# Performance work log

Hardware: AMD Instinct MI355X
Metric: run time of the kernel (lower is better)

Reference implementation:

```python
import jax, jax.numpy as jnp
import numpy as np

H = 128          # rnn_hid_size
SEQ_LEN = 2048
B = 4096
IN = 2           # SELECT_SIZE * 2


def _uniform(key, shape, stdv):
    return jax.random.uniform(key, shape, jnp.float32, -stdv, stdv)


def setup_inputs() -> dict:
    key = jax.random.key(0)
    ks = jax.random.split(key, 20)
    values = jax.random.normal(ks[0], (B, SEQ_LEN, 3), jnp.float32)
    masks = (jax.random.uniform(ks[1], (B, SEQ_LEN)) > 0.5).astype(jnp.float32)
    deltas = jax.random.uniform(ks[2], (B, SEQ_LEN, 3), jnp.float32)
    eval_masks = (jax.random.uniform(ks[3], (B, SEQ_LEN)) > 0.5).astype(jnp.float32)
    s = 1.0 / np.sqrt(H)
    params = {
        'Wih0': _uniform(ks[4], (4 * H, IN), s), 'Whh0': _uniform(ks[5], (4 * H, H), s),
        'bih0': _uniform(ks[6], (4 * H,), s), 'bhh0': _uniform(ks[7], (4 * H,), s),
        'Wih1': _uniform(ks[8], (4 * H, IN), s), 'Whh1': _uniform(ks[9], (4 * H, H), s),
        'bih1': _uniform(ks[10], (4 * H,), s), 'bhh1': _uniform(ks[11], (4 * H,), s),
        'td_W': _uniform(ks[12], (H, 1), s), 'td_b': _uniform(ks[13], (H,), s),
        'hr_W': _uniform(ks[14], (1, H), 1.0 / np.sqrt(H)), 'hr_b': _uniform(ks[15], (1,), 1.0 / np.sqrt(H)),
    }
    return dict(values=values, masks=masks, deltas=deltas, eval_masks=eval_masks, **params)


def _lstm_cell(x, h, c, Wih, Whh, bih, bhh):
    g = x @ Wih.T + bih + h @ Whh.T + bhh            # [B, 4H]
    i, f, gg, o = jnp.split(g, 4, axis=1)
    c2 = jax.nn.sigmoid(f) * c + jax.nn.sigmoid(i) * jnp.tanh(gg)
    h2 = jax.nn.sigmoid(o) * jnp.tanh(c2)
    return h2, c2


def reference(values, masks, deltas, eval_masks,
              Wih0, Whh0, bih0, bhh0, Wih1, Whh1, bih1, bhh1,
              td_W, td_b, hr_W, hr_b):
    bsize = values.shape[0]
    # time-major sequences for scan
    x_seq = jnp.transpose(values[:, :, 2:3], (1, 0, 2))      # [T, B, 1]
    m_seq = jnp.transpose(masks[:, :, None], (1, 0, 2))      # [T, B, 1]
    d_seq = jnp.transpose(deltas[:, :, 2:3], (1, 0, 2))      # [T, B, 1]
    in1_seq = jnp.transpose(values[:, :, 0:2], (1, 0, 2))    # [T, B, 2]

    h0 = jnp.zeros((bsize, H), jnp.float32)
    h1 = jnp.zeros((bsize, H), jnp.float32)
    c1 = jnp.zeros((bsize, H), jnp.float32)
    loss0 = jnp.zeros((), jnp.float32)

    def step(carry, inp):
        h0, h1, c1, loss = carry
        x_y, m_y, d_y, in1 = inp
        gamma_h = jnp.exp(-jax.nn.relu(d_y @ td_W.T + td_b))  # [B, H]
        x_h = h0 @ hr_W.T + hr_b                              # [B, 1]
        x_c = m_y * x_y + (1.0 - m_y) * x_h
        loss = loss + jnp.sum(jnp.square(x_y - x_h) * m_y) / (jnp.sum(m_y) + 1e-05)
        h1n, c1n = _lstm_cell(in1, h1, c1, Wih1, Whh1, bih1, bhh1)
        h1n = h1n * gamma_h
        inputs = jnp.concatenate([x_c, m_y], axis=1)          # [B, 2]
        h0n, _ = _lstm_cell(inputs, h1n, c1n, Wih0, Whh0, bih0, bhh0)
        return (h0n, h1n, c1n, loss), x_c

    (_, _, _, loss), imp = jax.lax.scan(step, (h0, h1, c1, loss0),
                                        (x_seq, m_seq, d_seq, in1_seq))
    imputations = jnp.transpose(imp, (1, 0, 2))               # [B, T, 1]
    evals = values[:, :, 2:3]
    return (loss, imputations, eval_masks[:, :, None], evals, masks[:, :, None])
```

## Files before the change

### kernel.cpp

```cpp
#include <hip/hip_runtime.h>

typedef __attribute__((ext_vector_type(8))) short bf16x8;
typedef __attribute__((ext_vector_type(4))) float f32x4;

#define L2E 1.4426950408889634f

__device__ __forceinline__ short f2bf(float x){
  unsigned u = __builtin_bit_cast(unsigned, x);
  u += 0x7fffu + ((u >> 16) & 1u);
  return (short)(u >> 16);
}
__device__ __forceinline__ float sigm(float x){
  float e = __builtin_amdgcn_exp2f(-x * L2E);
  return __builtin_amdgcn_rcpf(1.0f + e);
}
__device__ __forceinline__ float tanh_(float x){
  float e = __builtin_amdgcn_exp2f(x * (2.0f * L2E));
  return 1.0f - 2.0f * __builtin_amdgcn_rcpf(1.0f + e);
}

__device__ __forceinline__ void wg_barrier(){
  asm volatile("s_waitcnt lgkmcnt(0)" ::: "memory");
  __builtin_amdgcn_s_barrier();
  asm volatile("" ::: "memory");
}

__global__ __launch_bounds__(512, 2)
void rios_main(const float* __restrict__ values, const float* __restrict__ masks,
               const float* __restrict__ deltas,
               const float* __restrict__ Wih0, const float* __restrict__ Whh0,
               const float* __restrict__ bih0, const float* __restrict__ bhh0,
               const float* __restrict__ Wih1, const float* __restrict__ Whh1,
               const float* __restrict__ bih1, const float* __restrict__ bhh1,
               const float* __restrict__ td_W, const float* __restrict__ td_b,
               const float* __restrict__ hr_W, const float* __restrict__ hr_b,
               float* __restrict__ out, float* __restrict__ lossws)
{
  __shared__ short hb[2][16][136];
  __shared__ float xh_part[2][8][16];
  __shared__ float sA[2][5][16][16];
  __shared__ float xh_hist[16][16];

  const int tid = threadIdx.x;
  const int w  = tid >> 6;
  const int l  = tid & 63;
  const int q  = l >> 4;
  const int c  = l & 15;
  const int q4 = q << 2;
  const int u  = (w << 4) + c;
  const long long bb = (long long)blockIdx.x * 16;

  bf16x8 wf[2][4][4];
  {
    const float* WhhA[2] = { Whh1, Whh0 };
    #pragma unroll
    for (int cell = 0; cell < 2; ++cell)
      #pragma unroll
      for (int gi = 0; gi < 4; ++gi)
        #pragma unroll
        for (int kt = 0; kt < 4; ++kt){
          const float* rp = WhhA[cell] + (((gi << 7) + u) << 7) + (kt << 5) + (q << 3);
          bf16x8 f;
          #pragma unroll
          for (int j = 0; j < 8; ++j) f[j] = f2bf(rp[j]);
          wf[cell][gi][kt] = f;
        }
  }
  float wi[2][4][2], bs[2][4];
  {
    const float* WihA[2] = { Wih1, Wih0 };
    const float* bihA[2] = { bih1, bih0 };
    const float* bhhA[2] = { bhh1, bhh0 };
    #pragma unroll
    for (int cell = 0; cell < 2; ++cell)
      #pragma unroll
      for (int gi = 0; gi < 4; ++gi){
        int rg = (gi << 7) + u;
        wi[cell][gi][0] = WihA[cell][rg * 2];
        wi[cell][gi][1] = WihA[cell][rg * 2 + 1];
        bs[cell][gi]    = bihA[cell][rg] + bhhA[cell][rg];
      }
  }
  const float tdw = td_W[u], tdbv = td_b[u], hrw = hr_W[u], hrb = hr_b[0];

  {
    short* hz = &hb[0][0][0];
    for (int i = tid; i < 16 * 136; i += 512) hz[i] = 0;
    if (tid < 256) ((float*)xh_part)[tid] = 0.f;
  }

  const int isV = (tid < 192);
  const int isD = (tid >= 192 && tid < 384);
  const int isM = (tid >= 384 && tid < 448);
  int lb = 0, lp = 0;
  if (isV){ lb = tid / 12;        lp = tid % 12; }
  else if (isD){ lb = (tid-192)/12; lp = (tid-192)%12; }
  else if (isM){ lb = (tid-384)/4;  lp = (tid-384)%4; }
  const float* ldbase = nullptr;
  if (isV)      ldbase = values + ((bb + lb) * 2048LL) * 3 + lp * 4;
  else if (isD) ldbase = deltas + ((bb + lb) * 2048LL) * 3 + lp * 4;
  else if (isM) ldbase = masks  +  (bb + lb) * 2048LL      + lp * 4;

  auto write_stage = [&](int buf, f32x4 r){
    if (isV){
      #pragma unroll
      for (int j = 0; j < 4; ++j){ int idx = lp * 4 + j; sA[buf][idx % 3][idx / 3][lb] = r[j]; }
    } else if (isD){
      #pragma unroll
      for (int j = 0; j < 4; ++j){ int idx = lp * 4 + j; if (idx % 3 == 2) sA[buf][4][idx / 3][lb] = r[j]; }
    } else if (isM){
      #pragma unroll
      for (int j = 0; j < 4; ++j){ sA[buf][3][lp * 4 + j][lb] = r[j]; }
    }
  };

  if (tid < 448){
    f32x4 st = *(const f32x4*)(ldbase);
    write_stage(0, st);
  }
  __syncthreads();

  f32x4 c1 = {0.f, 0.f, 0.f, 0.f};

  for (int cc = 0; cc < 128; ++cc){
    const int cb = cc & 1;
    f32x4 nst;
    #pragma unroll 1
    for (int tt = 0; tt < 16; ++tt){
      const int s = (cc << 4) + tt;
      const int p = tt & 1;
      const int ob  = (tt == 0) ? (cb ^ 1) : cb;
      const int ott = (tt == 0) ? 15 : (tt - 1);

      if (w == 0 && tt == 1 && cc > 0){
        const int obase = (cc - 1) << 4;
        const int pb = cb ^ 1;
        const int m = l >> 2, j = l & 3;
        f32x4 st, wse, sm;
        #pragma unroll
        for (int k = 0; k < 4; ++k){
          const int t2 = (j << 2) + k;
          float xy2 = sA[pb][2][t2][m];
          float mm2 = sA[pb][3][t2][m];
          float xh2 = xh_hist[t2][m];
          st[k]  = mm2 * xy2 + (1.f - mm2) * xh2;
          float d2 = xy2 - xh2;
          wse[k] = d2 * d2 * mm2;
          sm[k]  = mm2;
        }
        *((f32x4*)&out[1 + (bb + m) * 2048LL + obase + (j << 2)]) = st;
        #pragma unroll
        for (int mk = 4; mk <= 32; mk <<= 1){
          #pragma unroll
          for (int k = 0; k < 4; ++k){ wse[k] += __shfl_xor(wse[k], mk); sm[k] += __shfl_xor(sm[k], mk); }
        }
        if (l < 4){
          #pragma unroll
          for (int k = 0; k < 4; ++k){
            atomicAdd(&lossws[((obase + (j << 2) + k) << 1)    ], wse[k]);
            atomicAdd(&lossws[((obase + (j << 2) + k) << 1) + 1], sm[k]);
          }
        }
      }

      f32x4 v0v = *(const f32x4*)&sA[cb][0][tt][q4];
      f32x4 v1v = *(const f32x4*)&sA[cb][1][tt][q4];
      f32x4 dv  = *(const f32x4*)&sA[cb][4][tt][q4];
      f32x4 acc[4];
      #pragma unroll
      for (int gi = 0; gi < 4; ++gi){
        #pragma unroll
        for (int r = 0; r < 4; ++r)
          acc[gi][r] = fmaf(v0v[r], wi[0][gi][0], fmaf(v1v[r], wi[0][gi][1], bs[0][gi]));
      }
      #pragma unroll
      for (int kt = 0; kt < 4; ++kt){
        bf16x8 af = *(const bf16x8*)&hb[p][c][(kt << 5) + (q << 3)];
        #pragma unroll
        for (int gi = 0; gi < 4; ++gi)
          acc[gi] = __builtin_amdgcn_mfma_f32_16x16x32_bf16(af, wf[0][gi][kt], acc[gi], 0, 0, 0);
      }

      f32x4 xh = { hrb, hrb, hrb, hrb };
      #pragma unroll
      for (int w2 = 0; w2 < 8; ++w2)
        xh += *(const f32x4*)&xh_part[p][w2][q4];
      f32x4 xy = *(const f32x4*)&sA[ob][2][ott][q4];
      f32x4 mm = *(const f32x4*)&sA[ob][3][ott][q4];
      f32x4 xcv = mm * xy + (1.f - mm) * xh;
      if (w == 0 && c == 0 && s > 0) *((f32x4*)&xh_hist[ott][q4]) = xh;

      f32x4 c_old = c1;
      #pragma unroll
      for (int r = 0; r < 4; ++r){
        float si = sigm(acc[0][r]);
        float sf = sigm(acc[1][r]);
        float tg = tanh_(acc[2][r]);
        float so = sigm(acc[3][r]);
        float c2 = sf * c1[r] + si * tg;
        float a1 = fmaxf(fmaf(dv[r], tdw, tdbv), 0.f);
        float gam = __builtin_amdgcn_exp2f(-a1 * L2E);
        c1[r] = c2;
        hb[p ^ 1][q4 + r][u] = f2bf(so * tanh_(c2) * gam);
      }

      #pragma unroll
      for (int gi = 0; gi < 4; ++gi){
        #pragma unroll
        for (int r = 0; r < 4; ++r)
          acc[gi][r] = fmaf(xcv[r], wi[1][gi][0], fmaf(mm[r], wi[1][gi][1], bs[1][gi]));
      }
      #pragma unroll
      for (int kt = 0; kt < 4; ++kt){
        bf16x8 af = *(const bf16x8*)&hb[p][c][(kt << 5) + (q << 3)];
        #pragma unroll
        for (int gi = 0; gi < 4; ++gi)
          acc[gi] = __builtin_amdgcn_mfma_f32_16x16x32_bf16(af, wf[1][gi][kt], acc[gi], 0, 0, 0);
      }
      f32x4 pv;
      #pragma unroll
      for (int r = 0; r < 4; ++r){
        float si = sigm(acc[0][r]);
        float sf = sigm(acc[1][r]);
        float tg = tanh_(acc[2][r]);
        float so = sigm(acc[3][r]);
        float c0n = sf * c_old[r] + si * tg;
        pv[r] = so * tanh_(c0n) * hrw;
      }
      #pragma unroll
      for (int mk = 1; mk < 16; mk <<= 1){
        #pragma unroll
        for (int r = 0; r < 4; ++r) pv[r] += __shfl_xor(pv[r], mk);
      }
      if (c == 0 && s > 0) *((f32x4*)&xh_part[p ^ 1][w][q4]) = pv;

      if (tt == 12 && cc + 1 < 128 && tid < 448){
        long long t0 = (long long)(cc + 1) * 16;
        nst = *(const f32x4*)(ldbase + (isM ? t0 : t0 * 3));
      }
      if (tt == 15 && cc + 1 < 128 && tid < 448) write_stage(cb ^ 1, nst);

      wg_barrier();
    }
  }

  if (w == 0){
    f32x4 xh = { hrb, hrb, hrb, hrb };
    #pragma unroll
    for (int w2 = 0; w2 < 8; ++w2)
      xh += *(const f32x4*)&xh_part[0][w2][q4];
    if (c == 0) *((f32x4*)&xh_hist[15][q4]) = xh;
    asm volatile("s_waitcnt lgkmcnt(0)" ::: "memory");
    const int obase = 2032;
    const int m = l >> 2, j = l & 3;
    f32x4 st, wse, sm;
    #pragma unroll
    for (int k = 0; k < 4; ++k){
      const int t2 = (j << 2) + k;
      float xy2 = sA[1][2][t2][m];
      float mm2 = sA[1][3][t2][m];
      float xh2 = xh_hist[t2][m];
      st[k]  = mm2 * xy2 + (1.f - mm2) * xh2;
      float d2 = xy2 - xh2;
      wse[k] = d2 * d2 * mm2;
      sm[k]  = mm2;
    }
    *((f32x4*)&out[1 + (bb + m) * 2048LL + obase + (j << 2)]) = st;
    #pragma unroll
    for (int mk = 4; mk <= 32; mk <<= 1){
      #pragma unroll
      for (int k = 0; k < 4; ++k){ wse[k] += __shfl_xor(wse[k], mk); sm[k] += __shfl_xor(sm[k], mk); }
    }
    if (l < 4){
      #pragma unroll
      for (int k = 0; k < 4; ++k){
        atomicAdd(&lossws[((obase + (j << 2) + k) << 1)    ], wse[k]);
        atomicAdd(&lossws[((obase + (j << 2) + k) << 1) + 1], sm[k]);
      }
    }
  }
}

__global__ void loss_reduce(const float* __restrict__ lossws, float* __restrict__ out){
  __shared__ float red[1024];
  int t = threadIdx.x;
  float v = lossws[2 * t] / (lossws[2 * t + 1] + 1e-5f)
          + lossws[2 * (t + 1024)] / (lossws[2 * (t + 1024) + 1] + 1e-5f);
  red[t] = v;
  __syncthreads();
  for (int s = 512; s > 0; s >>= 1){
    if (t < s) red[t] += red[t + s];
    __syncthreads();
  }
  if (t == 0) out[0] = red[0];
}

__global__ void copy_outs(const float* __restrict__ values, const float* __restrict__ masks,
                          const float* __restrict__ evalm, float* __restrict__ out){
  const long long M = 8388608LL;
  long long i = (long long)blockIdx.x * 256 + threadIdx.x;
  if (i < M){
    out[1 + M     + i] = evalm[i];
    out[1 + 2 * M + i] = values[3 * i + 2];
    out[1 + 3 * M + i] = masks[i];
  }
}

extern "C" void kernel_launch(void* const* d_in, const int* in_sizes, int n_in,
                              void* d_out, int out_size, void* d_ws, size_t ws_size,
                              hipStream_t stream){
  const float* values = (const float*)d_in[0];
  const float* masks  = (const float*)d_in[1];
  const float* deltas = (const float*)d_in[2];
  const float* evalm  = (const float*)d_in[3];
  const float* Wih0   = (const float*)d_in[4];
  const float* Whh0   = (const float*)d_in[5];
  const float* bih0   = (const float*)d_in[6];
  const float* bhh0   = (const float*)d_in[7];
  const float* Wih1   = (const float*)d_in[8];
  const float* Whh1   = (const float*)d_in[9];
  const float* bih1   = (const float*)d_in[10];
  const float* bhh1   = (const float*)d_in[11];
  const float* td_W   = (const float*)d_in[12];
  const float* td_b   = (const float*)d_in[13];
  const float* hr_W   = (const float*)d_in[14];
  const float* hr_b   = (const float*)d_in[15];
  float* out    = (float*)d_out;
  float* lossws = (float*)d_ws;

  hipMemsetAsync(lossws, 0, 2048 * 2 * sizeof(float), stream);
  hipLaunchKernelGGL(copy_outs, dim3(32768), dim3(256), 0, stream, values, masks, evalm, out);
  hipLaunchKernelGGL(rios_main, dim3(256), dim3(512), 0, stream,
                     values, masks, deltas, Wih0, Whh0, bih0, bhh0,
                     Wih1, Whh1, bih1, bhh1, td_W, td_b, hr_W, hr_b, out, lossws);
  hipLaunchKernelGGL(loss_reduce, dim3(1), dim3(1024), 0, stream, lossws, out);
}
```

Baseline: 10.13 ms.

## Split the two LSTM cells across separate wave groups running concurrently

The block grows to 1024 threads. Waves 0-7 now compute the time-decayed layer-1 cell and waves 8-15 compute the skewed layer-0 cell, instead of every wave doing both cells one after the other. The layer-1 cell state is passed through a new double-buffered LDS array so the other group can read it a step later. Each wave now holds only one cell's weight fragments, which lowers register pressure and halves the serial MFMA and transcendental chain per step. In exchange, twice as many waves join each per-step barrier, and the block's LDS footprint grows.

New measurement: 12.05 ms. +19.0%, slower.

```diff
diff --git a/kernel.cpp b/kernel.cpp
--- a/kernel.cpp
+++ b/kernel.cpp
@@ -25,7 +25,7 @@
   asm volatile("" ::: "memory");
 }
 
-__global__ __launch_bounds__(512, 2)
+__global__ __launch_bounds__(1024, 4)
 void rios_main(const float* __restrict__ values, const float* __restrict__ masks,
                const float* __restrict__ deltas,
                const float* __restrict__ Wih0, const float* __restrict__ Whh0,
@@ -37,55 +37,56 @@
                float* __restrict__ out, float* __restrict__ lossws)
 {
   __shared__ short hb[2][16][136];
+  __shared__ float cst[2][16][132];
   __shared__ float xh_part[2][8][16];
   __shared__ float sA[2][5][16][16];
   __shared__ float xh_hist[16][16];
 
   const int tid = threadIdx.x;
-  const int w  = tid >> 6;
-  const int l  = tid & 63;
-  const int q  = l >> 4;
-  const int c  = l & 15;
-  const int q4 = q << 2;
-  const int u  = (w << 4) + c;
+  const int w   = tid >> 6;
+  const int grp = w >> 3;
+  const int wg  = w & 7;
+  const int l   = tid & 63;
+  const int q   = l >> 4;
+  const int c   = l & 15;
+  const int q4  = q << 2;
+  const int u   = (wg << 4) + c;
   const long long bb = (long long)blockIdx.x * 16;
 
-  bf16x8 wf[2][4][4];
-  {
-    const float* WhhA[2] = { Whh1, Whh0 };
+  const float* Whh = grp == 0 ? Whh1 : Whh0;
+  const float* Wih = grp == 0 ? Wih1 : Wih0;
+  const float* bih = grp == 0 ? bih1 : bih0;
+  const float* bhh = grp == 0 ? bhh1 : bhh0;
+
+  bf16x8 wf[4][4];
+  #pragma unroll
+  for (int gi = 0; gi < 4; ++gi)
     #pragma unroll
-    for (int cell = 0; cell < 2; ++cell)
-      #pragma unroll
-      for (int gi = 0; gi < 4; ++gi)
-        #pragma unroll
-        for (int kt = 0; kt < 4; ++kt){
-          const float* rp = WhhA[cell] + (((gi << 7) + u) << 7) + (kt << 5) + (q << 3);
-          bf16x8 f;
-          #pragma unroll
-          for (int j = 0; j < 8; ++j) f[j] = f2bf(rp[j]);
-          wf[cell][gi][kt] = f;
-        }
-  }
-  float wi[2][4][2], bs[2][4];
-  {
-    const float* WihA[2] = { Wih1, Wih0 };
-    const float* bihA[2] = { bih1, bih0 };
-    const float* bhhA[2] = { bhh1, bhh0 };
-    #pragma unroll
-    for (int cell = 0; cell < 2; ++cell)
-      #pragma unroll
-      for (int gi = 0; gi < 4; ++gi){
-        int rg = (gi << 7) + u;
-        wi[cell][gi][0] = WihA[cell][rg * 2];
-        wi[cell][gi][1] = WihA[cell][rg * 2 + 1];
-        bs[cell][gi]    = bihA[cell][rg] + bhhA[cell][rg];
-      }
-  }
-  const float tdw = td_W[u], tdbv = td_b[u], hrw = hr_W[u], hrb = hr_b[0];
+    for (int kt = 0; kt < 4; ++kt){
+      const float* rp = Whh + (((gi << 7) + u) << 7) + (kt << 5) + (q << 3);
+      bf16x8 f;
+      #pragma unroll
+      for (int j = 0; j < 8; ++j) f[j] = f2bf(rp[j]);
+      wf[gi][kt] = f;
+    }
+  float wi[4][2], bs[4];
+  #pragma unroll
+  for (int gi = 0; gi < 4; ++gi){
+    int rg = (gi << 7) + u;
+    wi[gi][0] = Wih[rg * 2];
+    wi[gi][1] = Wih[rg * 2 + 1];
+    bs[gi]    = bih[rg] + bhh[rg];
+  }
+  float tdw = 0.f, tdbv = 0.f, hrw = 0.f;
+  if (grp == 0){ tdw = td_W[u]; tdbv = td_b[u]; }
+  else         { hrw = hr_W[u]; }
+  const float hrb = hr_b[0];
 
   {
     short* hz = &hb[0][0][0];
-    for (int i = tid; i < 16 * 136; i += 512) hz[i] = 0;
+    for (int i = tid; i < 16 * 136; i += 1024) hz[i] = 0;
+    float* cz = &cst[0][0][0];
+    for (int i = tid; i < 16 * 132; i += 1024) cz[i] = 0.f;
     if (tid < 256) ((float*)xh_part)[tid] = 0.f;
   }
 
@@ -132,107 +133,109 @@
       const int ob  = (tt == 0) ? (cb ^ 1) : cb;
       const int ott = (tt == 0) ? 15 : (tt - 1);
 
-      if (w == 0 && tt == 1 && cc > 0){
-        const int obase = (cc - 1) << 4;
-        const int pb = cb ^ 1;
-        const int m = l >> 2, j = l & 3;
-        f32x4 st, wse, sm;
-        #pragma unroll
-        for (int k = 0; k < 4; ++k){
-          const int t2 = (j << 2) + k;
-          float xy2 = sA[pb][2][t2][m];
-          float mm2 = sA[pb][3][t2][m];
-          float xh2 = xh_hist[t2][m];
-          st[k]  = mm2 * xy2 + (1.f - mm2) * xh2;
-          float d2 = xy2 - xh2;
-          wse[k] = d2 * d2 * mm2;
-          sm[k]  = mm2;
-        }
-        *((f32x4*)&out[1 + (bb + m) * 2048LL + obase + (j << 2)]) = st;
-        #pragma unroll
-        for (int mk = 4; mk <= 32; mk <<= 1){
-          #pragma unroll
-          for (int k = 0; k < 4; ++k){ wse[k] += __shfl_xor(wse[k], mk); sm[k] += __shfl_xor(sm[k], mk); }
-        }
-        if (l < 4){
+      if (grp == 0){
+        f32x4 v0v = *(const f32x4*)&sA[cb][0][tt][q4];
+        f32x4 v1v = *(const f32x4*)&sA[cb][1][tt][q4];
+        f32x4 dv  = *(const f32x4*)&sA[cb][4][tt][q4];
+        f32x4 acc[4];
+        #pragma unroll
+        for (int gi = 0; gi < 4; ++gi){
+          #pragma unroll
+          for (int r = 0; r < 4; ++r)
+            acc[gi][r] = fmaf(v0v[r], wi[gi][0], fmaf(v1v[r], wi[gi][1], bs[gi]));
+        }
+        #pragma unroll
+        for (int kt = 0; kt < 4; ++kt){
+          bf16x8 af = *(const bf16x8*)&hb[p][c][(kt << 5) + (q << 3)];
+          #pragma unroll
+          for (int gi = 0; gi < 4; ++gi)
+            acc[gi] = __builtin_amdgcn_mfma_f32_16x16x32_bf16(af, wf[gi][kt], acc[gi], 0, 0, 0);
+        }
+        #pragma unroll
+        for (int r = 0; r < 4; ++r){
+          float si = sigm(acc[0][r]);
+          float sf = sigm(acc[1][r]);
+          float tg = tanh_(acc[2][r]);
+          float so = sigm(acc[3][r]);
+          float c2 = sf * c1[r] + si * tg;
+          float a1 = fmaxf(fmaf(dv[r], tdw, tdbv), 0.f);
+          float gam = __builtin_amdgcn_exp2f(-a1 * L2E);
+          c1[r] = c2;
+          hb [p ^ 1][q4 + r][u] = f2bf(so * tanh_(c2) * gam);
+          cst[p ^ 1][q4 + r][u] = c2;
+        }
+      } else {
+        if (w == 15 && tt == 1 && cc > 0){
+          const int obase = (cc - 1) << 4;
+          const int pb = cb ^ 1;
+          const int m = l >> 2, j = l & 3;
+          f32x4 st, wse, sm;
           #pragma unroll
           for (int k = 0; k < 4; ++k){
-            atomicAdd(&lossws[((obase + (j << 2) + k) << 1)    ], wse[k]);
-            atomicAdd(&lossws[((obase + (j << 2) + k) << 1) + 1], sm[k]);
+            const int t2 = (j << 2) + k;
+            float xy2 = sA[pb][2][t2][m];
+            float mm2 = sA[pb][3][t2][m];
+            float xh2 = xh_hist[t2][m];
+            st[k]  = mm2 * xy2 + (1.f - mm2) * xh2;
+            float d2 = xy2 - xh2;
+            wse[k] = d2 * d2 * mm2;
+            sm[k]  = mm2;
           }
-        }
+          *((f32x4*)&out[1 + (bb + m) * 2048LL + obase + (j << 2)]) = st;
+          #pragma unroll
+          for (int mk = 4; mk <= 32; mk <<= 1){
+            #pragma unroll
+            for (int k = 0; k < 4; ++k){ wse[k] += __shfl_xor(wse[k], mk); sm[k] += __shfl_xor(sm[k], mk); }
+          }
+          if (l < 4){
+            #pragma unroll
+            for (int k = 0; k < 4; ++k){
+              atomicAdd(&lossws[((obase + (j << 2) + k) << 1)    ], wse[k]);
+              atomicAdd(&lossws[((obase + (j << 2) + k) << 1) + 1], sm[k]);
+            }
+          }
+        }
+
+        f32x4 xh = { hrb, hrb, hrb, hrb };
+        #pragma unroll
+        for (int w2 = 0; w2 < 8; ++w2)
+          xh += *(const f32x4*)&xh_part[p][w2][q4];
+        f32x4 xy = *(const f32x4*)&sA[ob][2][ott][q4];
+        f32x4 mm = *(const f32x4*)&sA[ob][3][ott][q4];
+        f32x4 xcv = mm * xy + (1.f - mm) * xh;
+        if (w == 8 && c == 0 && s > 0) *((f32x4*)&xh_hist[ott][q4]) = xh;
+
+        f32x4 acc[4];
+        #pragma unroll
+        for (int gi = 0; gi < 4; ++gi){
+          #pragma unroll
+          for (int r = 0; r < 4; ++r)
+            acc[gi][r] = fmaf(xcv[r], wi[gi][0], fmaf(mm[r], wi[gi][1], bs[gi]));
+        }
+        #pragma unroll
+        for (int kt = 0; kt < 4; ++kt){
+          bf16x8 af = *(const bf16x8*)&hb[p][c][(kt << 5) + (q << 3)];
+          #pragma unroll
+          for (int gi = 0; gi < 4; ++gi)
+            acc[gi] = __builtin_amdgcn_mfma_f32_16x16x32_bf16(af, wf[gi][kt], acc[gi], 0, 0, 0);
+        }
+        f32x4 pv;
+        #pragma unroll
+        for (int r = 0; r < 4; ++r){
+          float si = sigm(acc[0][r]);
+          float sf = sigm(acc[1][r]);
+          float tg = tanh_(acc[2][r]);
+          float so = sigm(acc[3][r]);
+          float c0n = sf * cst[p][q4 + r][u] + si * tg;
+          pv[r] = so * tanh_(c0n) * hrw;
+        }
+        #pragma unroll
+        for (int mk = 1; mk < 16; mk <<= 1){
+          #pragma unroll
+          for (int r = 0; r < 4; ++r) pv[r] += __shfl_xor(pv[r], mk);
+        }
+        if (c == 0 && s > 0) *((f32x4*)&xh_part[p ^ 1][wg][q4]) = pv;
       }
-
-      f32x4 v0v = *(const f32x4*)&sA[cb][0][tt][q4];
-      f32x4 v1v = *(const f32x4*)&sA[cb][1][tt][q4];
-      f32x4 dv  = *(const f32x4*)&sA[cb][4][tt][q4];
-      f32x4 acc[4];
-      #pragma unroll
-      for (int gi = 0; gi < 4; ++gi){
-        #pragma unroll
-        for (int r = 0; r < 4; ++r)
-          acc[gi][r] = fmaf(v0v[r], wi[0][gi][0], fmaf(v1v[r], wi[0][gi][1], bs[0][gi]));
-      }
-      #pragma unroll
-      for (int kt = 0; kt < 4; ++kt){
-        bf16x8 af = *(const bf16x8*)&hb[p][c][(kt << 5) + (q << 3)];
-        #pragma unroll
-        for (int gi = 0; gi < 4; ++gi)
-          acc[gi] = __builtin_amdgcn_mfma_f32_16x16x32_bf16(af, wf[0][gi][kt], acc[gi], 0, 0, 0);
-      }
-
-      f32x4 xh = { hrb, hrb, hrb, hrb };
-      #pragma unroll
-      for (int w2 = 0; w2 < 8; ++w2)
-        xh += *(const f32x4*)&xh_part[p][w2][q4];
-      f32x4 xy = *(const f32x4*)&sA[ob][2][ott][q4];
-      f32x4 mm = *(const f32x4*)&sA[ob][3][ott][q4];
-      f32x4 xcv = mm * xy + (1.f - mm) * xh;
-      if (w == 0 && c == 0 && s > 0) *((f32x4*)&xh_hist[ott][q4]) = xh;
-
-      f32x4 c_old = c1;
-      #pragma unroll
-      for (int r = 0; r < 4; ++r){
-        float si = sigm(acc[0][r]);
-        float sf = sigm(acc[1][r]);
-        float tg = tanh_(acc[2][r]);
-        float so = sigm(acc[3][r]);
-        float c2 = sf * c1[r] + si * tg;
-        float a1 = fmaxf(fmaf(dv[r], tdw, tdbv), 0.f);
-        float gam = __builtin_amdgcn_exp2f(-a1 * L2E);
-        c1[r] = c2;
-        hb[p ^ 1][q4 + r][u] = f2bf(so * tanh_(c2) * gam);
-      }
-
-      #pragma unroll
-      for (int gi = 0; gi < 4; ++gi){
-        #pragma unroll
-        for (int r = 0; r < 4; ++r)
-          acc[gi][r] = fmaf(xcv[r], wi[1][gi][0], fmaf(mm[r], wi[1][gi][1], bs[1][gi]));
-      }
-      #pragma unroll
-      for (int kt = 0; kt < 4; ++kt){
-        bf16x8 af = *(const bf16x8*)&hb[p][c][(kt << 5) + (q << 3)];
-        #pragma unroll
-        for (int gi = 0; gi < 4; ++gi)
-          acc[gi] = __builtin_amdgcn_mfma_f32_16x16x32_bf16(af, wf[1][gi][kt], acc[gi], 0, 0, 0);
-      }
-      f32x4 pv;
-      #pragma unroll
-      for (int r = 0; r < 4; ++r){
-        float si = sigm(acc[0][r]);
-        float sf = sigm(acc[1][r]);
-        float tg = tanh_(acc[2][r]);
-        float so = sigm(acc[3][r]);
-        float c0n = sf * c_old[r] + si * tg;
-        pv[r] = so * tanh_(c0n) * hrw;
-      }
-      #pragma unroll
-      for (int mk = 1; mk < 16; mk <<= 1){
-        #pragma unroll
-        for (int r = 0; r < 4; ++r) pv[r] += __shfl_xor(pv[r], mk);
-      }
-      if (c == 0 && s > 0) *((f32x4*)&xh_part[p ^ 1][w][q4]) = pv;
 
       if (tt == 12 && cc + 1 < 128 && tid < 448){
         long long t0 = (long long)(cc + 1) * 16;
@@ -244,13 +247,15 @@
     }
   }
 
-  if (w == 0){
+  if (w == 8){
     f32x4 xh = { hrb, hrb, hrb, hrb };
     #pragma unroll
     for (int w2 = 0; w2 < 8; ++w2)
       xh += *(const f32x4*)&xh_part[0][w2][q4];
     if (c == 0) *((f32x4*)&xh_hist[15][q4]) = xh;
-    asm volatile("s_waitcnt lgkmcnt(0)" ::: "memory");
+  }
+  wg_barrier();
+  if (w == 15){
     const int obase = 2032;
     const int m = l >> 2, j = l & 3;
     f32x4 st, wse, sm;
@@ -330,7 +335,7 @@
 
   hipMemsetAsync(lossws, 0, 2048 * 2 * sizeof(float), stream);
   hipLaunchKernelGGL(copy_outs, dim3(32768), dim3(256), 0, stream, values, masks, evalm, out);
-  hipLaunchKernelGGL(rios_main, dim3(256), dim3(512), 0, stream,
+  hipLaunchKernelGGL(rios_main, dim3(256), dim3(1024), 0, stream,
                      values, masks, deltas, Wih0, Whh0, bih0, bhh0,
                      Wih1, Whh1, bih1, bhh1, td_W, td_b, hr_W, hr_b, out, lossws);
   hipLaunchKernelGGL(loss_reduce, dim3(1), dim3(1024), 0, stream, lossws, out);
```

## De-skew LSTM cell pipeline with mid-step barrier and DPP row reductions

Applied to the files above, without the earlier changes.

Removes the one-step skew between the two LSTM cells: cell1 writes h1, a workgroup barrier follows, then cell0 reads the fresh h1 in the same step, so the partial-sum and staging buffers can be single-buffered. The 16-lane shuffle reduction for the hr projection becomes a DPP row_shr reduction, the tail and loss work moves to wave 7, and the inner loop is unrolled by 2. The aim is simpler indexing and cheaper cross-lane sums. In exchange it adds a second barrier per timestep and serializes the two cells' MFMA chains, which removes the overlap the skewed schedule had.

New measurement: 9.106 ms. 1.11x faster.

```diff
diff --git a/kernel.cpp b/kernel.cpp
--- a/kernel.cpp
+++ b/kernel.cpp
@@ -17,6 +17,23 @@
 __device__ __forceinline__ float tanh_(float x){
   float e = __builtin_amdgcn_exp2f(x * (2.0f * L2E));
   return 1.0f - 2.0f * __builtin_amdgcn_rcpf(1.0f + e);
+}
+
+template<int CTRL>
+__device__ __forceinline__ float dpp_add(float v){
+  int s = __builtin_amdgcn_mov_dpp(__builtin_bit_cast(int, v), CTRL, 0xf, 0xf, true);
+  return v + __builtin_bit_cast(float, s);
+}
+__device__ __forceinline__ void row_sum16(f32x4& pv){
+  #pragma unroll
+  for (int r = 0; r < 4; ++r){
+    float v = pv[r];
+    v = dpp_add<0x121>(v);
+    v = dpp_add<0x122>(v);
+    v = dpp_add<0x124>(v);
+    v = dpp_add<0x128>(v);
+    pv[r] = v;
+  }
 }
 
 __device__ __forceinline__ void wg_barrier(){
@@ -37,9 +54,9 @@
                float* __restrict__ out, float* __restrict__ lossws)
 {
   __shared__ short hb[2][16][136];
-  __shared__ float xh_part[2][8][16];
+  __shared__ float xh_part[8][16];
   __shared__ float sA[2][5][16][16];
-  __shared__ float xh_hist[16][16];
+  __shared__ float xh_hist[2][16][16];
 
   const int tid = threadIdx.x;
   const int w  = tid >> 6;
@@ -86,7 +103,7 @@
   {
     short* hz = &hb[0][0][0];
     for (int i = tid; i < 16 * 136; i += 512) hz[i] = 0;
-    if (tid < 256) ((float*)xh_part)[tid] = 0.f;
+    if (tid < 128) ((float*)xh_part)[tid] = 0.f;
   }
 
   const int isV = (tid < 192);
@@ -125,14 +142,11 @@
   for (int cc = 0; cc < 128; ++cc){
     const int cb = cc & 1;
     f32x4 nst;
-    #pragma unroll 1
+    #pragma unroll 2
     for (int tt = 0; tt < 16; ++tt){
-      const int s = (cc << 4) + tt;
       const int p = tt & 1;
-      const int ob  = (tt == 0) ? (cb ^ 1) : cb;
-      const int ott = (tt == 0) ? 15 : (tt - 1);
-
-      if (w == 0 && tt == 1 && cc > 0){
+
+      if (w == 7 && tt == 1 && cc > 0){
         const int obase = (cc - 1) << 4;
         const int pb = cb ^ 1;
         const int m = l >> 2, j = l & 3;
@@ -142,7 +156,7 @@
           const int t2 = (j << 2) + k;
           float xy2 = sA[pb][2][t2][m];
           float mm2 = sA[pb][3][t2][m];
-          float xh2 = xh_hist[t2][m];
+          float xh2 = xh_hist[pb][t2][m];
           st[k]  = mm2 * xy2 + (1.f - mm2) * xh2;
           float d2 = xy2 - xh2;
           wse[k] = d2 * d2 * mm2;
@@ -166,6 +180,15 @@
       f32x4 v0v = *(const f32x4*)&sA[cb][0][tt][q4];
       f32x4 v1v = *(const f32x4*)&sA[cb][1][tt][q4];
       f32x4 dv  = *(const f32x4*)&sA[cb][4][tt][q4];
+      f32x4 xh = { hrb, hrb, hrb, hrb };
+      #pragma unroll
+      for (int w2 = 0; w2 < 8; ++w2)
+        xh += *(const f32x4*)&xh_part[w2][q4];
+      f32x4 xy = *(const f32x4*)&sA[cb][2][tt][q4];
+      f32x4 mm = *(const f32x4*)&sA[cb][3][tt][q4];
+      f32x4 xcv = mm * xy + (1.f - mm) * xh;
+      if (w == 0 && c == 0) *((f32x4*)&xh_hist[cb][tt][q4]) = xh;
+
       f32x4 acc[4];
       #pragma unroll
       for (int gi = 0; gi < 4; ++gi){
@@ -180,17 +203,6 @@
         for (int gi = 0; gi < 4; ++gi)
           acc[gi] = __builtin_amdgcn_mfma_f32_16x16x32_bf16(af, wf[0][gi][kt], acc[gi], 0, 0, 0);
       }
-
-      f32x4 xh = { hrb, hrb, hrb, hrb };
-      #pragma unroll
-      for (int w2 = 0; w2 < 8; ++w2)
-        xh += *(const f32x4*)&xh_part[p][w2][q4];
-      f32x4 xy = *(const f32x4*)&sA[ob][2][ott][q4];
-      f32x4 mm = *(const f32x4*)&sA[ob][3][ott][q4];
-      f32x4 xcv = mm * xy + (1.f - mm) * xh;
-      if (w == 0 && c == 0 && s > 0) *((f32x4*)&xh_hist[ott][q4]) = xh;
-
-      f32x4 c_old = c1;
       #pragma unroll
       for (int r = 0; r < 4; ++r){
         float si = sigm(acc[0][r]);
@@ -200,9 +212,11 @@
         float c2 = sf * c1[r] + si * tg;
         float a1 = fmaxf(fmaf(dv[r], tdw, tdbv), 0.f);
         float gam = __builtin_amdgcn_exp2f(-a1 * L2E);
+        float h1n = so * tanh_(c2) * gam;
         c1[r] = c2;
-        hb[p ^ 1][q4 + r][u] = f2bf(so * tanh_(c2) * gam);
-      }
+        hb[p ^ 1][q4 + r][u] = f2bf(h1n);
+      }
+      wg_barrier();
 
       #pragma unroll
       for (int gi = 0; gi < 4; ++gi){
@@ -212,7 +226,7 @@
       }
       #pragma unroll
       for (int kt = 0; kt < 4; ++kt){
-        bf16x8 af = *(const bf16x8*)&hb[p][c][(kt << 5) + (q << 3)];
+        bf16x8 af = *(const bf16x8*)&hb[p ^ 1][c][(kt << 5) + (q << 3)];
         #pragma unroll
         for (int gi = 0; gi < 4; ++gi)
           acc[gi] = __builtin_amdgcn_mfma_f32_16x16x32_bf16(af, wf[1][gi][kt], acc[gi], 0, 0, 0);
@@ -224,15 +238,12 @@
         float sf = sigm(acc[1][r]);
         float tg = tanh_(acc[2][r]);
         float so = sigm(acc[3][r]);
-        float c0n = sf * c_old[r] + si * tg;
-        pv[r] = so * tanh_(c0n) * hrw;
-      }
-      #pragma unroll
-      for (int mk = 1; mk < 16; mk <<= 1){
-        #pragma unroll
-        for (int r = 0; r < 4; ++r) pv[r] += __shfl_xor(pv[r], mk);
-      }
-      if (c == 0 && s > 0) *((f32x4*)&xh_part[p ^ 1][w][q4]) = pv;
+        float c0n = sf * c1[r] + si * tg;
+        float h0n = so * tanh_(c0n);
+        pv[r] = h0n * hrw;
+      }
+      row_sum16(pv);
+      if (c == 0) *((f32x4*)&xh_part[w][q4]) = pv;
 
       if (tt == 12 && cc + 1 < 128 && tid < 448){
         long long t0 = (long long)(cc + 1) * 16;
@@ -244,13 +255,7 @@
     }
   }
 
-  if (w == 0){
-    f32x4 xh = { hrb, hrb, hrb, hrb };
-    #pragma unroll
-    for (int w2 = 0; w2 < 8; ++w2)
-      xh += *(const f32x4*)&xh_part[0][w2][q4];
-    if (c == 0) *((f32x4*)&xh_hist[15][q4]) = xh;
-    asm volatile("s_waitcnt lgkmcnt(0)" ::: "memory");
+  if (w == 7){
     const int obase = 2032;
     const int m = l >> 2, j = l & 3;
     f32x4 st, wse, sm;
@@ -259,7 +264,7 @@
       const int t2 = (j << 2) + k;
       float xy2 = sA[1][2][t2][m];
       float mm2 = sA[1][3][t2][m];
-      float xh2 = xh_hist[t2][m];
+      float xh2 = xh_hist[1][t2][m];
       st[k]  = mm2 * xy2 + (1.f - mm2) * xh2;
       float d2 = xy2 - xh2;
       wse[k] = d2 * d2 * mm2;
```
